# Optimization experiments

Hardware: AMD Instinct MI355X
Metric: run time of the kernel (lower is better)

## Reference

```python
import jax, jax.numpy as jnp
import numpy as np

B, N, K, D = 8, 4096, 8, 256
EPS = 1e-8
LN_EPS = 1e-5


def setup_inputs() -> dict:
    key = jax.random.key(0)
    ks = jax.random.split(key, 9)
    lim_s = float(np.sqrt(6.0 / (K + D)))   # xavier_uniform on (K, D) fan dims
    lim_w = float(np.sqrt(6.0 / (D + D)))   # xavier-ish init for square Linear weights
    return {
        "embeddings": jax.random.normal(ks[0], (B, N, D), jnp.float32),
        "slots_mu": jax.random.uniform(ks[1], (1, K, D), jnp.float32, -lim_s, lim_s),
        "slots_logsigma": jax.random.uniform(ks[2], (1, K, D), jnp.float32, -lim_s, lim_s),
        "mixing_coeffs": jnp.full((1, K), 1.0 / K, jnp.float32),
        "Wq": jax.random.uniform(ks[3], (D, D), jnp.float32, -lim_w, lim_w),
        "Wk": jax.random.uniform(ks[4], (D, D), jnp.float32, -lim_w, lim_w),
        "Wv": jax.random.uniform(ks[5], (D, D), jnp.float32, -lim_w, lim_w),
        "ln_scale": jnp.ones((D,), jnp.float32),
        "ln_bias": jnp.zeros((D,), jnp.float32),
        "noise_init": jax.random.normal(ks[6], (B, K, D), jnp.float32),
        "noise_final": jax.random.normal(ks[7], (B, K, D), jnp.float32),
        "num_iterations": 3,
    }


def _layer_norm(x, scale, bias):
    m = jnp.mean(x, axis=-1, keepdims=True)
    v = jnp.mean((x - m) ** 2, axis=-1, keepdims=True)  # biased var, matches torch LayerNorm
    return (x - m) / jnp.sqrt(v + LN_EPS) * scale + bias


def reference(embeddings, slots_mu, slots_logsigma, mixing_coeffs, Wq, Wk, Wv,
              ln_scale, ln_bias, noise_init, noise_final, num_iterations):
    b, n, d = embeddings.shape
    k = slots_mu.shape[1]
    mix = jnp.broadcast_to(mixing_coeffs, (b, k))               # (B,K)
    mu = jnp.broadcast_to(slots_mu, (b, k, d))                  # (B,K,D)
    sigma = jnp.exp(jnp.broadcast_to(slots_logsigma, (b, k, d)))
    slots = mu + sigma * noise_init                             # slots never updated in loop (faithful)

    x = _layer_norm(embeddings, ln_scale, ln_bias)
    keys = x @ Wk.T                                             # (B,N,D)
    values = x @ Wv.T                                           # (B,N,D)

    log_norm_const = jnp.float32(-0.5 * d * np.log(2.0 * np.pi))
    attn = None
    for _ in range(num_iterations):
        queries = slots @ Wq.T                                  # (B,K,D)
        diff = keys[:, :, None, :] - queries[:, None, :, :]     # (B,N,K,D)
        gll = -0.5 * jnp.sum(diff ** 2 / (sigma[:, None] ** 2 + EPS), axis=-1)  # (B,N,K)
        gll = (log_norm_const
               - 0.5 * jnp.sum(jnp.log(jnp.abs(sigma) + EPS), axis=-1)[:, None, :]
               + gll)
        gll = jnp.clip(gll, -10000.0, 10000.0)
        log_attn = jnp.log(mix + EPS)[:, None, :] + gll         # (B,N,K)
        attn = jax.nn.softmax(log_attn, axis=1)                 # softmax over N
        mu = jnp.einsum('bnk,bnd->bkd', attn, values)           # weighted mean
        diff_v = values[:, :, None, :] - mu[:, None, :, :]      # (B,N,K,D)
        sigma = jnp.einsum('bnk,bnkd->bkd', attn, diff_v ** 2)  # weighted variance
        mix = jnp.sum(attn, axis=1) / n

    sigma = jnp.maximum(jnp.abs(sigma), EPS)
    slots_out = mu + sigma * noise_final
    return slots_out, jnp.transpose(attn, (0, 2, 1))            # (B,K,D), (B,K,N)
```

## Files before the change

### kernel.cpp

```cpp
#include <hip/hip_runtime.h>
#include <math.h>


#define Bd 8
#define Nd 4096
#define Kd 8
#define Dd 256
#define Md (Bd*Nd)
#define NITER 3
#define EPSf 1e-8f
#define LNEPS 1e-5f
#define NCH 64
#define LOGNORM -235.24826450039617f

typedef float f32x4 __attribute__((ext_vector_type(4)));
typedef short bf16x8 __attribute__((ext_vector_type(8)));
typedef unsigned short ushort_t;
typedef unsigned short us4 __attribute__((ext_vector_type(4)));

#define KEYS_OFF 0
#define VALS_OFF (Md*Dd)
#define E_OFF    (2*Md*Dd)
#define Q_OFF    (E_OFF + Bd*Kd*Nd)
#define W_OFF    (Q_OFF + Bd*Kd*Dd)
#define CST_OFF  (W_OFF + Bd*Kd*Dd)
#define MSP_OFF  (CST_OFF + 64)
#define SSP_OFF  (MSP_OFF + Bd*Kd*NCH)
#define PMU_OFF  (SSP_OFF + Bd*Kd*NCH)
#define PS2_OFF  (PMU_OFF + Bd*NCH*Kd*Dd)
#define WH_OFF   (PS2_OFF + Bd*NCH*Kd*Dd)
#define WL_OFF   (WH_OFF + 65536)
#define XH_OFF   (WL_OFF + 65536)
#define XL_OFF   (XH_OFF + Md*Dd/2)
#define WS_TOTAL (XL_OFF + Md*Dd/2)

__device__ __forceinline__ ushort_t f2bf(float f) {
    unsigned u = __float_as_uint(f);
    return (ushort_t)((u + 0x7FFFu + ((u >> 16) & 1u)) >> 16);
}
__device__ __forceinline__ float b2f(ushort_t h) {
    return __uint_as_float(((unsigned)h) << 16);
}
__device__ __forceinline__ void gload_lds16(const void* g, void* l) {
    __builtin_amdgcn_global_load_lds(
        (__attribute__((address_space(1))) void*)g,
        (__attribute__((address_space(3))) void*)l, 16, 0, 0);
}

__global__ __launch_bounds__(256) void k_setup(
        const float* __restrict__ emb, const float* __restrict__ lns,
        const float* __restrict__ lnb, const float* __restrict__ Wk,
        const float* __restrict__ Wv, const float* __restrict__ mu0,
        const float* __restrict__ lsig, const float* __restrict__ nz0,
        const float* __restrict__ Wq, ushort_t* __restrict__ xh,
        ushort_t* __restrict__ xl, ushort_t* __restrict__ Wh,
        ushort_t* __restrict__ Wl, float* __restrict__ qout,
        float* __restrict__ w_ws, float* __restrict__ cst_ws) {
    __shared__ float s_s[256];
    __shared__ float red[256];
    const int bx = blockIdx.x;
    if (bx < 1024) {
        const int tid = threadIdx.x, wave = tid >> 6, lane = tid & 63;
        const int row0 = bx * 32;
        const float4 sc = ((const float4*)lns)[lane];
        const float4 bi = ((const float4*)lnb)[lane];
        for (int rr = 0; rr < 8; ++rr) {
            const int r = row0 + wave * 8 + rr;
            const float4 e4 = ((const float4*)(emb + (size_t)r * Dd))[lane];
            float s = e4.x + e4.y + e4.z + e4.w;
            #pragma unroll
            for (int off = 32; off; off >>= 1) s += __shfl_xor(s, off);
            const float m = s * (1.0f / 256.0f);
            const float dx = e4.x - m, dy = e4.y - m, dz = e4.z - m, dw = e4.w - m;
            float ss = dx * dx + dy * dy + dz * dz + dw * dw;
            #pragma unroll
            for (int off = 32; off; off >>= 1) ss += __shfl_xor(ss, off);
            const float rs = 1.0f / sqrtf(ss * (1.0f / 256.0f) + LNEPS);
            float x[4];
            x[0] = dx * rs * sc.x + bi.x;
            x[1] = dy * rs * sc.y + bi.y;
            x[2] = dz * rs * sc.z + bi.z;
            x[3] = dw * rs * sc.w + bi.w;
            us4 h4, l4;
            #pragma unroll
            for (int j = 0; j < 4; ++j) {
                const ushort_t h = f2bf(x[j]);
                h4[j] = h;
                l4[j] = f2bf(x[j] - b2f(h));
            }
            *(us4*)(xh + (size_t)r * Dd + lane * 4) = h4;
            *(us4*)(xl + (size_t)r * Dd + lane * 4) = l4;
        }
    } else if (bx < 1536) {
        const int r = bx - 1024, d = threadIdx.x;
        const float w = (r < 256) ? Wk[(size_t)r * 256 + d]
                                  : Wv[(size_t)(r - 256) * 256 + d];
        const ushort_t h = f2bf(w);
        Wh[(size_t)r * 256 + d] = h;
        Wl[(size_t)r * 256 + d] = f2bf(w - b2f(h));
    } else {
        const int bk = bx - 1536;
        const int k = bk & 7;
        const int d = threadIdx.x;
        const float sg = expf(lsig[k * 256 + d]);
        s_s[d] = mu0[k * 256 + d] + sg * nz0[(size_t)bk * 256 + d];
        w_ws[(size_t)bk * 256 + d] = 1.0f / (sg * sg + EPSf);
        red[d] = logf(fabsf(sg) + EPSf);
        __syncthreads();
        for (int s = 128; s; s >>= 1) {
            if (d < s) red[d] += red[d + s];
            __syncthreads();
        }
        if (d == 0) cst_ws[bk] = LOGNORM - 0.5f * red[0];
        float acc = 0.0f;
        const float4* Wr = (const float4*)(Wq + (size_t)d * 256);
        const float4* sp = (const float4*)s_s;
        #pragma unroll 8
        for (int j = 0; j < 64; ++j) {
            const float4 w4 = Wr[j], s4 = sp[j];
            acc += w4.x * s4.x + w4.y * s4.y + w4.z * s4.z + w4.w * s4.w;
        }
        qout[(size_t)bk * 256 + d] = acc;
    }
}

__global__ __launch_bounds__(256, 2) void k_gemm(
        const ushort_t* __restrict__ xh, const ushort_t* __restrict__ xl,
        const ushort_t* __restrict__ Wh, const ushort_t* __restrict__ Wl,
        float* __restrict__ keys, float* __restrict__ vals) {
    __shared__ ushort_t Ah[128 * 32], Al[128 * 32];
    __shared__ ushort_t Bh[256 * 32], Bl[256 * 32];
    const int tid = threadIdx.x, lane = tid & 63, wave = tid >> 6;
    const int row0 = blockIdx.x * 128;
    const int cb = blockIdx.y;
    const int wm = wave >> 1, wn = wave & 1;

    f32x4 acc[4][8];
    #pragma unroll
    for (int a = 0; a < 4; ++a)
        #pragma unroll
        for (int b = 0; b < 8; ++b) acc[a][b] = (f32x4)(0.0f);

    for (int jb = 0; jb < 256; jb += 32) {
        #pragma unroll
        for (int i = 0; i < 2; ++i) {
            const int p = tid + i * 256;
            const int r = p >> 2, gp = p & 3;
            const int g = gp ^ ((r >> 1) & 3);
            const size_t goff = (size_t)(row0 + r) * 256 + jb + g * 8;
            gload_lds16(xh + goff, &Ah[p * 8]);
            gload_lds16(xl + goff, &Al[p * 8]);
        }
        #pragma unroll
        for (int i = 0; i < 4; ++i) {
            const int p = (wave * 4 + i) * 64 + lane;
            const int r = p >> 2, gp = p & 3;
            const int g = gp ^ ((r >> 1) & 3);
            const size_t goff = (size_t)(cb * 256 + r) * 256 + jb + g * 8;
            gload_lds16(Wh + goff, &Bh[p * 8]);
            gload_lds16(Wl + goff, &Bl[p * 8]);
        }
        __syncthreads();

        bf16x8 bhf[8], blf[8];
        #pragma unroll
        for (int ni = 0; ni < 8; ++ni) {
            const int c = wn * 128 + ni * 16 + (lane & 15);
            const int g = lane >> 4;
            const int off = c * 32 + ((g ^ ((c >> 1) & 3)) << 3);
            bhf[ni] = *(const bf16x8*)&Bh[off];
            blf[ni] = *(const bf16x8*)&Bl[off];
        }
        #pragma unroll
        for (int mi = 0; mi < 4; ++mi) {
            const int rr = wm * 64 + mi * 16 + (lane & 15);
            const int g = lane >> 4;
            const int off = rr * 32 + ((g ^ ((rr >> 1) & 3)) << 3);
            const bf16x8 ah = *(const bf16x8*)&Ah[off];
            const bf16x8 al = *(const bf16x8*)&Al[off];
            #pragma unroll
            for (int ni = 0; ni < 8; ++ni) {
                acc[mi][ni] = __builtin_amdgcn_mfma_f32_16x16x32_bf16(ah, bhf[ni], acc[mi][ni], 0, 0, 0);
                acc[mi][ni] = __builtin_amdgcn_mfma_f32_16x16x32_bf16(ah, blf[ni], acc[mi][ni], 0, 0, 0);
                acc[mi][ni] = __builtin_amdgcn_mfma_f32_16x16x32_bf16(al, bhf[ni], acc[mi][ni], 0, 0, 0);
            }
        }
        __syncthreads();
    }
    float* outp = (cb == 0) ? keys : vals;
    #pragma unroll
    for (int mi = 0; mi < 4; ++mi) {
        const int rbase = row0 + wm * 64 + mi * 16 + ((lane >> 4) << 2);
        #pragma unroll
        for (int ni = 0; ni < 8; ++ni) {
            const int col = wn * 128 + ni * 16 + (lane & 15);
            #pragma unroll
            for (int rg = 0; rg < 4; ++rg)
                outp[(size_t)(rbase + rg) * Dd + col] = acc[mi][ni][rg];
        }
    }
}

__global__ __launch_bounds__(512, 4) void k_fuse(
        const float* __restrict__ keys, const float* __restrict__ vals,
        const float* __restrict__ q_ws, const float* __restrict__ w_ws,
        const float* __restrict__ cst_ws, float* __restrict__ e_glob,
        float* __restrict__ msp, float* __restrict__ ssp,
        float* __restrict__ pmu, float* __restrict__ ps2, const int last) {
    __shared__ float buf[16384];
    __shared__ float e_s[8][64];
    const int tid = threadIdx.x, lane = tid & 63, wv = tid >> 6;
    const int b = blockIdx.x >> 6, chunk = blockIdx.x & 63;
    const int n0 = chunk * 64;
    const int wvu = __builtin_amdgcn_readfirstlane(wv);

    const float* kbase = keys + ((size_t)b * Nd + n0) * Dd;
    #pragma unroll
    for (int i = 0; i < 8; ++i) {
        const int p = i * 512 + tid;
        const int row = p >> 6, gp = p & 63;
        const int g = gp ^ row;
        gload_lds16(kbase + (size_t)row * Dd + g * 4, &buf[p * 4]);
    }
    __syncthreads();

    const float4* qk = (const float4*)(q_ws + ((size_t)b * Kd + wvu) * Dd);
    const float4* wk = (const float4*)(w_ws + ((size_t)b * Kd + wvu) * Dd);
    const float* krow = &buf[lane * 256];
    float ax = 0.f, ay = 0.f, az = 0.f, aw = 0.f;
    #pragma unroll 8
    for (int g = 0; g < 64; ++g) {
        const float4 k4 = *(const float4*)&krow[(g ^ lane) * 4];
        const float4 q4 = qk[g];
        const float4 w4 = wk[g];
        float t;
        t = k4.x - q4.x; ax += t * t * w4.x;
        t = k4.y - q4.y; ay += t * t * w4.y;
        t = k4.z - q4.z; az += t * t * w4.z;
        t = k4.w - q4.w; aw += t * t * w4.w;
    }
    float gv = cst_ws[b * Kd + wvu] - 0.5f * ((ax + ay) + (az + aw));
    gv = fminf(fmaxf(gv, -10000.0f), 10000.0f);
    float m = gv;
    #pragma unroll
    for (int off = 32; off; off >>= 1) m = fmaxf(m, __shfl_xor(m, off));
    const float e = expf(gv - m);
    float ssum = e;
    #pragma unroll
    for (int off = 32; off; off >>= 1) ssum += __shfl_xor(ssum, off);
    e_s[wv][lane] = e;
    if (last) e_glob[((size_t)(b * Kd + wvu)) * Nd + n0 + lane] = e;
    if (lane == 0) {
        msp[(b * Kd + wvu) * NCH + chunk] = m;
        ssp[(b * Kd + wvu) * NCH + chunk] = ssum;
    }
    __syncthreads();

    const float* vbase = vals + ((size_t)b * Nd + n0) * Dd;
    #pragma unroll
    for (int i = 0; i < 8; ++i) {
        const int p = i * 512 + tid;
        gload_lds16(vbase + (size_t)p * 4, &buf[p * 4]);
    }
    __syncthreads();

    float4 mu4 = {0.f, 0.f, 0.f, 0.f}, s24 = {0.f, 0.f, 0.f, 0.f};
    #pragma unroll 8
    for (int n = 0; n < 64; ++n) {
        const float4 v = *(const float4*)&buf[n * 256 + lane * 4];
        const float a = e_s[wv][n];
        mu4.x += a * v.x; mu4.y += a * v.y; mu4.z += a * v.z; mu4.w += a * v.w;
        s24.x += a * v.x * v.x; s24.y += a * v.y * v.y;
        s24.z += a * v.z * v.z; s24.w += a * v.w * v.w;
    }
    const size_t o = (((size_t)(b * NCH + chunk)) * Kd + wv) * Dd + lane * 4;
    *(float4*)(pmu + o) = mu4;
    *(float4*)(ps2 + o) = s24;
}

__global__ __launch_bounds__(256) void k_prep(
        const float* __restrict__ msp, const float* __restrict__ ssp,
        const float* __restrict__ pmu, const float* __restrict__ ps2,
        float* __restrict__ w_ws, float* __restrict__ cst_ws,
        const float* __restrict__ nzf, float* __restrict__ slots_out,
        const float* __restrict__ e_glob, float* __restrict__ attn,
        const int last) {
    __shared__ float wS[64];
    __shared__ float aS[64];
    __shared__ float sinv_s;
    __shared__ float4 muP[4][64];
    __shared__ float4 s2P[4][64];
    const int bk = blockIdx.x;
    const int b = bk >> 3, k = bk & 7;
    const int tid = threadIdx.x, lane = tid & 63, grp = tid >> 6;
    if (grp == 0) {
        const float m_c = msp[bk * NCH + lane];
        const float s_c = ssp[bk * NCH + lane];
        float M = m_c;
        #pragma unroll
        for (int off = 32; off; off >>= 1) M = fmaxf(M, __shfl_xor(M, off));
        const float wc = expf(m_c - M);
        float S = wc * s_c;
        #pragma unroll
        for (int off = 32; off; off >>= 1) S += __shfl_xor(S, off);
        wS[lane] = wc;
        aS[lane] = wc / S;
        if (lane == 0) sinv_s = 1.0f / S;
    }
    __syncthreads();
    float4 am = {0.f, 0.f, 0.f, 0.f}, a2 = {0.f, 0.f, 0.f, 0.f};
    #pragma unroll
    for (int i = 0; i < 16; ++i) {
        const int c = grp * 16 + i;
        const float wc = wS[c];
        const size_t o = (((size_t)(b * NCH + c)) * Kd + k) * Dd + lane * 4;
        const float4 pm = *(const float4*)(pmu + o);
        const float4 p2 = *(const float4*)(ps2 + o);
        am.x += wc * pm.x; am.y += wc * pm.y; am.z += wc * pm.z; am.w += wc * pm.w;
        a2.x += wc * p2.x; a2.y += wc * p2.y; a2.z += wc * p2.z; a2.w += wc * p2.w;
    }
    muP[grp][lane] = am;
    s2P[grp][lane] = a2;
    __syncthreads();
    if (grp == 0) {
        const float sinv = sinv_s;
        float4 mu, E2;
        mu.x = (muP[0][lane].x + muP[1][lane].x + muP[2][lane].x + muP[3][lane].x) * sinv;
        mu.y = (muP[0][lane].y + muP[1][lane].y + muP[2][lane].y + muP[3][lane].y) * sinv;
        mu.z = (muP[0][lane].z + muP[1][lane].z + muP[2][lane].z + muP[3][lane].z) * sinv;
        mu.w = (muP[0][lane].w + muP[1][lane].w + muP[2][lane].w + muP[3][lane].w) * sinv;
        E2.x = (s2P[0][lane].x + s2P[1][lane].x + s2P[2][lane].x + s2P[3][lane].x) * sinv;
        E2.y = (s2P[0][lane].y + s2P[1][lane].y + s2P[2][lane].y + s2P[3][lane].y) * sinv;
        E2.z = (s2P[0][lane].z + s2P[1][lane].z + s2P[2][lane].z + s2P[3][lane].z) * sinv;
        E2.w = (s2P[0][lane].w + s2P[1][lane].w + s2P[2][lane].w + s2P[3][lane].w) * sinv;
        float4 sg;
        sg.x = E2.x - mu.x * mu.x; sg.y = E2.y - mu.y * mu.y;
        sg.z = E2.z - mu.z * mu.z; sg.w = E2.w - mu.w * mu.w;
        float4 wout;
        wout.x = 1.0f / (sg.x * sg.x + EPSf); wout.y = 1.0f / (sg.y * sg.y + EPSf);
        wout.z = 1.0f / (sg.z * sg.z + EPSf); wout.w = 1.0f / (sg.w * sg.w + EPSf);
        *(float4*)(w_ws + (size_t)bk * Dd + lane * 4) = wout;
        const float4 nz = *(const float4*)(nzf + (size_t)bk * Dd + lane * 4);
        float4 so;
        so.x = mu.x + fmaxf(fabsf(sg.x), EPSf) * nz.x;
        so.y = mu.y + fmaxf(fabsf(sg.y), EPSf) * nz.y;
        so.z = mu.z + fmaxf(fabsf(sg.z), EPSf) * nz.z;
        so.w = mu.w + fmaxf(fabsf(sg.w), EPSf) * nz.w;
        *(float4*)(slots_out + (size_t)bk * Dd + lane * 4) = so;
        float lsum = logf(fabsf(sg.x) + EPSf) + logf(fabsf(sg.y) + EPSf)
                   + logf(fabsf(sg.z) + EPSf) + logf(fabsf(sg.w) + EPSf);
        #pragma unroll
        for (int off = 32; off; off >>= 1) lsum += __shfl_xor(lsum, off);
        if (lane == 0) cst_ws[bk] = LOGNORM - 0.5f * lsum;
    }
    if (last) {
        const float4* erow = (const float4*)(e_glob + (size_t)bk * Nd);
        float4* arow = (float4*)(attn + (size_t)bk * Nd);
        #pragma unroll
        for (int i = 0; i < 4; ++i) {
            const int idx = tid + i * 256;
            const float4 e4 = erow[idx];
            const float a = aS[idx >> 4];
            float4 o4;
            o4.x = e4.x * a; o4.y = e4.y * a; o4.z = e4.z * a; o4.w = e4.w * a;
            arow[idx] = o4;
        }
    }
}

extern "C" void kernel_launch(void* const* d_in, const int* in_sizes, int n_in,
                              void* d_out, int out_size, void* d_ws, size_t ws_size,
                              hipStream_t stream) {
    const float* emb  = (const float*)d_in[0];
    const float* mu0  = (const float*)d_in[1];
    const float* lsig = (const float*)d_in[2];
    const float* Wq   = (const float*)d_in[4];
    const float* Wk   = (const float*)d_in[5];
    const float* Wv   = (const float*)d_in[6];
    const float* lns  = (const float*)d_in[7];
    const float* lnb  = (const float*)d_in[8];
    const float* nz0  = (const float*)d_in[9];
    const float* nzf  = (const float*)d_in[10];

    float* ws    = (float*)d_ws;
    float* out   = (float*)d_out;
    float* keys  = ws + KEYS_OFF;
    float* vals  = ws + VALS_OFF;
    float* eglob = ws + E_OFF;
    float* qws   = ws + Q_OFF;
    float* wws   = ws + W_OFF;
    float* cstw  = ws + CST_OFF;
    float* msp   = ws + MSP_OFF;
    float* ssp   = ws + SSP_OFF;
    float* pmu   = ws + PMU_OFF;
    float* ps2   = ws + PS2_OFF;
    ushort_t* Whp = (ushort_t*)(ws + WH_OFF);
    ushort_t* Wlp = (ushort_t*)(ws + WL_OFF);
    ushort_t* xhp = (ushort_t*)(ws + XH_OFF);
    ushort_t* xlp = (ushort_t*)(ws + XL_OFF);
    float* attn = out + Bd * Kd * Dd;

    k_setup<<<1600, 256, 0, stream>>>(emb, lns, lnb, Wk, Wv, mu0, lsig, nz0,
                                      Wq, xhp, xlp, Whp, Wlp, qws, wws, cstw);
    k_gemm<<<dim3(256, 2), 256, 0, stream>>>(xhp, xlp, Whp, Wlp, keys, vals);
    for (int it = 0; it < NITER; ++it) {
        const int last = (it == NITER - 1);
        k_fuse<<<512, 512, 0, stream>>>(keys, vals, qws, wws, cstw, eglob,
                                        msp, ssp, pmu, ps2, last);
        k_prep<<<64, 256, 0, stream>>>(msp, ssp, pmu, ps2, wws, cstw, nzf,
                                       out, eglob, attn, last);
    }
    (void)in_sizes; (void)n_in; (void)out_size; (void)ws_size;
}
```

Baseline: 208.2 us.

## Split per-slot reduction kernel across D-slices with atomic log-sum accumulation

The reduction kernel that combines per-chunk softmax partials into mu, sigma and the log-normalizer now runs as 512 blocks of 512 threads instead of 64 blocks of 256. Each block handles one 32-wide D slice of a (b,k) slot and reduces chunks with wave shuffles. Because the log-sum constant now spans several blocks, it is accumulated with atomicAdd into a per-iteration buffer that setup zeroes, and the fuse kernel reads it. Slot outputs are written only on the last iteration. This raises parallelism in a kernel that previously filled few CUs, at the cost of atomics and repeated per-block max/scale computation.

```diff
diff --git a/kernel.cpp b/kernel.cpp
--- a/kernel.cpp
+++ b/kernel.cpp
@@ -24,7 +24,8 @@
 #define Q_OFF    (E_OFF + Bd*Kd*Nd)
 #define W_OFF    (Q_OFF + Bd*Kd*Dd)
 #define CST_OFF  (W_OFF + Bd*Kd*Dd)
-#define MSP_OFF  (CST_OFF + 64)
+#define CSTA_OFF (CST_OFF + 64)
+#define MSP_OFF  (CSTA_OFF + 192)
 #define SSP_OFF  (MSP_OFF + Bd*Kd*NCH)
 #define PMU_OFF  (SSP_OFF + Bd*Kd*NCH)
 #define PS2_OFF  (PMU_OFF + Bd*NCH*Kd*Dd)
@@ -55,7 +56,8 @@
         const float* __restrict__ Wq, ushort_t* __restrict__ xh,
         ushort_t* __restrict__ xl, ushort_t* __restrict__ Wh,
         ushort_t* __restrict__ Wl, float* __restrict__ qout,
-        float* __restrict__ w_ws, float* __restrict__ cst_ws) {
+        float* __restrict__ w_ws, float* __restrict__ cst_ws,
+        float* __restrict__ cst_acc) {
     __shared__ float s_s[256];
     __shared__ float red[256];
     const int bx = blockIdx.x;
@@ -102,6 +104,7 @@
         const int bk = bx - 1536;
         const int k = bk & 7;
         const int d = threadIdx.x;
+        if (d < 3) cst_acc[d * 64 + bk] = 0.0f;
         const float sg = expf(lsig[k * 256 + d]);
         s_s[d] = mu0[k * 256 + d] + sg * nz0[(size_t)bk * 256 + d];
         w_ws[(size_t)bk * 256 + d] = 1.0f / (sg * sg + EPSf);
@@ -204,9 +207,10 @@
 __global__ __launch_bounds__(512, 4) void k_fuse(
         const float* __restrict__ keys, const float* __restrict__ vals,
         const float* __restrict__ q_ws, const float* __restrict__ w_ws,
-        const float* __restrict__ cst_ws, float* __restrict__ e_glob,
-        float* __restrict__ msp, float* __restrict__ ssp,
-        float* __restrict__ pmu, float* __restrict__ ps2, const int last) {
+        const float* __restrict__ cst_ws, const float* __restrict__ cst_acc,
+        float* __restrict__ e_glob, float* __restrict__ msp,
+        float* __restrict__ ssp, float* __restrict__ pmu,
+        float* __restrict__ ps2, const int it, const int last) {
     __shared__ float buf[16384];
     __shared__ float e_s[8][64];
     const int tid = threadIdx.x, lane = tid & 63, wv = tid >> 6;
@@ -224,8 +228,11 @@
     }
     __syncthreads();
 
-    const float4* qk = (const float4*)(q_ws + ((size_t)b * Kd + wvu) * Dd);
-    const float4* wk = (const float4*)(w_ws + ((size_t)b * Kd + wvu) * Dd);
+    const int bkf = b * Kd + wvu;
+    const float4* qk = (const float4*)(q_ws + (size_t)bkf * Dd);
+    const float4* wk = (const float4*)(w_ws + (size_t)bkf * Dd);
+    const float cstv = (it == 0) ? cst_ws[bkf]
+                     : fmaf(-0.5f, cst_acc[(it - 1) * 64 + bkf], LOGNORM);
     const float* krow = &buf[lane * 256];
     float ax = 0.f, ay = 0.f, az = 0.f, aw = 0.f;
     #pragma unroll 8
@@ -239,7 +246,7 @@
         t = k4.z - q4.z; az += t * t * w4.z;
         t = k4.w - q4.w; aw += t * t * w4.w;
     }
-    float gv = cst_ws[b * Kd + wvu] - 0.5f * ((ax + ay) + (az + aw));
+    float gv = cstv - 0.5f * ((ax + ay) + (az + aw));
     gv = fminf(fmaxf(gv, -10000.0f), 10000.0f);
     float m = gv;
     #pragma unroll
@@ -249,10 +256,10 @@
     #pragma unroll
     for (int off = 32; off; off >>= 1) ssum += __shfl_xor(ssum, off);
     e_s[wv][lane] = e;
-    if (last) e_glob[((size_t)(b * Kd + wvu)) * Nd + n0 + lane] = e;
+    if (last) e_glob[((size_t)bkf) * Nd + n0 + lane] = e;
     if (lane == 0) {
-        msp[(b * Kd + wvu) * NCH + chunk] = m;
-        ssp[(b * Kd + wvu) * NCH + chunk] = ssum;
+        msp[bkf * NCH + chunk] = m;
+        ssp[bkf * NCH + chunk] = ssum;
     }
     __syncthreads();
 
@@ -278,22 +285,21 @@
     *(float4*)(ps2 + o) = s24;
 }
 
-__global__ __launch_bounds__(256) void k_prep(
+__global__ __launch_bounds__(512) void k_red(
         const float* __restrict__ msp, const float* __restrict__ ssp,
         const float* __restrict__ pmu, const float* __restrict__ ps2,
-        float* __restrict__ w_ws, float* __restrict__ cst_ws,
+        float* __restrict__ w_ws, float* __restrict__ cst_acc,
         const float* __restrict__ nzf, float* __restrict__ slots_out,
         const float* __restrict__ e_glob, float* __restrict__ attn,
-        const int last) {
-    __shared__ float wS[64];
+        const int it, const int last) {
     __shared__ float aS[64];
-    __shared__ float sinv_s;
-    __shared__ float4 muP[4][64];
-    __shared__ float4 s2P[4][64];
-    const int bk = blockIdx.x;
+    __shared__ f32x4 redm[8][8], red2[8][8];
+    const int bx = blockIdx.x;
+    const int bk = bx >> 3, ds = bx & 7;
     const int b = bk >> 3, k = bk & 7;
-    const int tid = threadIdx.x, lane = tid & 63, grp = tid >> 6;
-    if (grp == 0) {
+    const int tid = threadIdx.x, lane = tid & 63, wv = tid >> 6;
+
+    if (wv == 0) {
         const float m_c = msp[bk * NCH + lane];
         const float s_c = ssp[bk * NCH + lane];
         float M = m_c;
@@ -303,68 +309,72 @@
         float S = wc * s_c;
         #pragma unroll
         for (int off = 32; off; off >>= 1) S += __shfl_xor(S, off);
-        wS[lane] = wc;
         aS[lane] = wc / S;
-        if (lane == 0) sinv_s = 1.0f / S;
     }
     __syncthreads();
-    float4 am = {0.f, 0.f, 0.f, 0.f}, a2 = {0.f, 0.f, 0.f, 0.f};
-    #pragma unroll
-    for (int i = 0; i < 16; ++i) {
-        const int c = grp * 16 + i;
-        const float wc = wS[c];
-        const size_t o = (((size_t)(b * NCH + c)) * Kd + k) * Dd + lane * 4;
-        const float4 pm = *(const float4*)(pmu + o);
-        const float4 p2 = *(const float4*)(ps2 + o);
-        am.x += wc * pm.x; am.y += wc * pm.y; am.z += wc * pm.z; am.w += wc * pm.w;
-        a2.x += wc * p2.x; a2.y += wc * p2.y; a2.z += wc * p2.z; a2.w += wc * p2.w;
-    }
-    muP[grp][lane] = am;
-    s2P[grp][lane] = a2;
+
+    const int c0 = tid >> 3, f = tid & 7;
+    const size_t base = (((size_t)(b * NCH + c0)) * Kd + k) * Dd + ds * 32 + f * 4;
+    const float a = aS[c0];
+    const float4 pm = *(const float4*)(pmu + base);
+    const float4 p2 = *(const float4*)(ps2 + base);
+    f32x4 m4 = {a * pm.x, a * pm.y, a * pm.z, a * pm.w};
+    f32x4 e4 = {a * p2.x, a * p2.y, a * p2.z, a * p2.w};
+    #pragma unroll
+    for (int off = 8; off < 64; off <<= 1) {
+        m4.x += __shfl_xor(m4.x, off); m4.y += __shfl_xor(m4.y, off);
+        m4.z += __shfl_xor(m4.z, off); m4.w += __shfl_xor(m4.w, off);
+        e4.x += __shfl_xor(e4.x, off); e4.y += __shfl_xor(e4.y, off);
+        e4.z += __shfl_xor(e4.z, off); e4.w += __shfl_xor(e4.w, off);
+    }
+    if (lane < 8) { redm[wv][lane] = m4; red2[wv][lane] = e4; }
     __syncthreads();
-    if (grp == 0) {
-        const float sinv = sinv_s;
-        float4 mu, E2;
-        mu.x = (muP[0][lane].x + muP[1][lane].x + muP[2][lane].x + muP[3][lane].x) * sinv;
-        mu.y = (muP[0][lane].y + muP[1][lane].y + muP[2][lane].y + muP[3][lane].y) * sinv;
-        mu.z = (muP[0][lane].z + muP[1][lane].z + muP[2][lane].z + muP[3][lane].z) * sinv;
-        mu.w = (muP[0][lane].w + muP[1][lane].w + muP[2][lane].w + muP[3][lane].w) * sinv;
-        E2.x = (s2P[0][lane].x + s2P[1][lane].x + s2P[2][lane].x + s2P[3][lane].x) * sinv;
-        E2.y = (s2P[0][lane].y + s2P[1][lane].y + s2P[2][lane].y + s2P[3][lane].y) * sinv;
-        E2.z = (s2P[0][lane].z + s2P[1][lane].z + s2P[2][lane].z + s2P[3][lane].z) * sinv;
-        E2.w = (s2P[0][lane].w + s2P[1][lane].w + s2P[2][lane].w + s2P[3][lane].w) * sinv;
-        float4 sg;
-        sg.x = E2.x - mu.x * mu.x; sg.y = E2.y - mu.y * mu.y;
-        sg.z = E2.z - mu.z * mu.z; sg.w = E2.w - mu.w * mu.w;
-        float4 wout;
-        wout.x = 1.0f / (sg.x * sg.x + EPSf); wout.y = 1.0f / (sg.y * sg.y + EPSf);
-        wout.z = 1.0f / (sg.z * sg.z + EPSf); wout.w = 1.0f / (sg.w * sg.w + EPSf);
-        *(float4*)(w_ws + (size_t)bk * Dd + lane * 4) = wout;
-        const float4 nz = *(const float4*)(nzf + (size_t)bk * Dd + lane * 4);
-        float4 so;
-        so.x = mu.x + fmaxf(fabsf(sg.x), EPSf) * nz.x;
-        so.y = mu.y + fmaxf(fabsf(sg.y), EPSf) * nz.y;
-        so.z = mu.z + fmaxf(fabsf(sg.z), EPSf) * nz.z;
-        so.w = mu.w + fmaxf(fabsf(sg.w), EPSf) * nz.w;
-        *(float4*)(slots_out + (size_t)bk * Dd + lane * 4) = so;
-        float lsum = logf(fabsf(sg.x) + EPSf) + logf(fabsf(sg.y) + EPSf)
-                   + logf(fabsf(sg.z) + EPSf) + logf(fabsf(sg.w) + EPSf);
-        #pragma unroll
-        for (int off = 32; off; off >>= 1) lsum += __shfl_xor(lsum, off);
-        if (lane == 0) cst_ws[bk] = LOGNORM - 0.5f * lsum;
-    }
-    if (last) {
-        const float4* erow = (const float4*)(e_glob + (size_t)bk * Nd);
-        float4* arow = (float4*)(attn + (size_t)bk * Nd);
-        #pragma unroll
-        for (int i = 0; i < 4; ++i) {
-            const int idx = tid + i * 256;
-            const float4 e4 = erow[idx];
-            const float a = aS[idx >> 4];
-            float4 o4;
-            o4.x = e4.x * a; o4.y = e4.y * a; o4.z = e4.z * a; o4.w = e4.w * a;
-            arow[idx] = o4;
-        }
+
+    if (wv == 0) {
+        f32x4 mm = redm[lane >> 3][lane & 7];
+        f32x4 ee = red2[lane >> 3][lane & 7];
+        #pragma unroll
+        for (int off = 8; off < 64; off <<= 1) {
+            mm.x += __shfl_xor(mm.x, off); mm.y += __shfl_xor(mm.y, off);
+            mm.z += __shfl_xor(mm.z, off); mm.w += __shfl_xor(mm.w, off);
+            ee.x += __shfl_xor(ee.x, off); ee.y += __shfl_xor(ee.y, off);
+            ee.z += __shfl_xor(ee.z, off); ee.w += __shfl_xor(ee.w, off);
+        }
+        if (lane < 8) {
+            const int d0 = ds * 32 + lane * 4;
+            const float sgx = ee.x - mm.x * mm.x;
+            const float sgy = ee.y - mm.y * mm.y;
+            const float sgz = ee.z - mm.z * mm.z;
+            const float sgw = ee.w - mm.w * mm.w;
+            float4 wout;
+            wout.x = 1.0f / (sgx * sgx + EPSf);
+            wout.y = 1.0f / (sgy * sgy + EPSf);
+            wout.z = 1.0f / (sgz * sgz + EPSf);
+            wout.w = 1.0f / (sgw * sgw + EPSf);
+            *(float4*)(w_ws + (size_t)bk * Dd + d0) = wout;
+            if (last) {
+                const float4 nz = *(const float4*)(nzf + (size_t)bk * Dd + d0);
+                float4 so;
+                so.x = mm.x + fmaxf(fabsf(sgx), EPSf) * nz.x;
+                so.y = mm.y + fmaxf(fabsf(sgy), EPSf) * nz.y;
+                so.z = mm.z + fmaxf(fabsf(sgz), EPSf) * nz.z;
+                so.w = mm.w + fmaxf(fabsf(sgw), EPSf) * nz.w;
+                *(float4*)(slots_out + (size_t)bk * Dd + d0) = so;
+            }
+            float ls = logf(fabsf(sgx) + EPSf) + logf(fabsf(sgy) + EPSf)
+                     + logf(fabsf(sgz) + EPSf) + logf(fabsf(sgw) + EPSf);
+            #pragma unroll
+            for (int off = 1; off < 8; off <<= 1) ls += __shfl_xor(ls, off);
+            if (lane == 0) atomicAdd(cst_acc + it * 64 + bk, ls);
+        }
+    }
+    if (last && tid < 128) {
+        const int idx = ds * 128 + tid;
+        const float4 ev = ((const float4*)(e_glob + (size_t)bk * Nd))[idx];
+        const float s = aS[idx >> 4];
+        float4 o4;
+        o4.x = ev.x * s; o4.y = ev.y * s; o4.z = ev.z * s; o4.w = ev.w * s;
+        ((float4*)(attn + (size_t)bk * Nd))[idx] = o4;
     }
 }
 
@@ -390,6 +400,7 @@
     float* qws   = ws + Q_OFF;
     float* wws   = ws + W_OFF;
     float* cstw  = ws + CST_OFF;
+    float* csta  = ws + CSTA_OFF;
     float* msp   = ws + MSP_OFF;
     float* ssp   = ws + SSP_OFF;
     float* pmu   = ws + PMU_OFF;
@@ -401,14 +412,15 @@
     float* attn = out + Bd * Kd * Dd;
 
     k_setup<<<1600, 256, 0, stream>>>(emb, lns, lnb, Wk, Wv, mu0, lsig, nz0,
-                                      Wq, xhp, xlp, Whp, Wlp, qws, wws, cstw);
+                                      Wq, xhp, xlp, Whp, Wlp, qws, wws, cstw,
+                                      csta);
     k_gemm<<<dim3(256, 2), 256, 0, stream>>>(xhp, xlp, Whp, Wlp, keys, vals);
     for (int it = 0; it < NITER; ++it) {
         const int last = (it == NITER - 1);
-        k_fuse<<<512, 512, 0, stream>>>(keys, vals, qws, wws, cstw, eglob,
-                                        msp, ssp, pmu, ps2, last);
-        k_prep<<<64, 256, 0, stream>>>(msp, ssp, pmu, ps2, wws, cstw, nzf,
-                                       out, eglob, attn, last);
+        k_fuse<<<512, 512, 0, stream>>>(keys, vals, qws, wws, cstw, csta,
+                                        eglob, msp, ssp, pmu, ps2, it, last);
+        k_red<<<512, 512, 0, stream>>>(msp, ssp, pmu, ps2, wws, csta, nzf,
+                                       out, eglob, attn, it, last);
     }
     (void)in_sizes; (void)n_in; (void)out_size; (void)ws_size;
 }
```

After: 215.3 us. 3.4% more time.

## Read values directly from global in fused kernel; widen prep kernel to 1024 threads

Applied to the files above, without the earlier changes.

In the fused attention kernel, the LDS staging of the value tile and its two barriers are removed, and each wave reads values straight from global memory with coalesced float4 loads. The reduction kernel grows from 256 to 1024 threads per block, so each of 16 groups reduces 4 chunk partials instead of 4 groups reducing 16, and the attention normalization becomes a single float4 per thread. The aim is to cut barrier and LDS-copy latency and to expose more parallelism in the small 64-block prep kernel. The cost is that the 8 waves of a block each reread the same value tile from global or L2 instead of sharing one LDS copy, and the final cross-group sum is longer.

```diff
diff --git a/kernel.cpp b/kernel.cpp
--- a/kernel.cpp
+++ b/kernel.cpp
@@ -254,20 +254,12 @@
         msp[(b * Kd + wvu) * NCH + chunk] = m;
         ssp[(b * Kd + wvu) * NCH + chunk] = ssum;
     }
-    __syncthreads();
-
-    const float* vbase = vals + ((size_t)b * Nd + n0) * Dd;
-    #pragma unroll
-    for (int i = 0; i < 8; ++i) {
-        const int p = i * 512 + tid;
-        gload_lds16(vbase + (size_t)p * 4, &buf[p * 4]);
-    }
-    __syncthreads();
 
     float4 mu4 = {0.f, 0.f, 0.f, 0.f}, s24 = {0.f, 0.f, 0.f, 0.f};
+    const float* vbase = vals + ((size_t)b * Nd + n0) * Dd + lane * 4;
     #pragma unroll 8
     for (int n = 0; n < 64; ++n) {
-        const float4 v = *(const float4*)&buf[n * 256 + lane * 4];
+        const float4 v = *(const float4*)(vbase + (size_t)n * Dd);
         const float a = e_s[wv][n];
         mu4.x += a * v.x; mu4.y += a * v.y; mu4.z += a * v.z; mu4.w += a * v.w;
         s24.x += a * v.x * v.x; s24.y += a * v.y * v.y;
@@ -278,7 +270,7 @@
     *(float4*)(ps2 + o) = s24;
 }
 
-__global__ __launch_bounds__(256) void k_prep(
+__global__ __launch_bounds__(1024) void k_prep(
         const float* __restrict__ msp, const float* __restrict__ ssp,
         const float* __restrict__ pmu, const float* __restrict__ ps2,
         float* __restrict__ w_ws, float* __restrict__ cst_ws,
@@ -288,8 +280,8 @@
     __shared__ float wS[64];
     __shared__ float aS[64];
     __shared__ float sinv_s;
-    __shared__ float4 muP[4][64];
-    __shared__ float4 s2P[4][64];
+    __shared__ float4 muP[16][64];
+    __shared__ float4 s2P[16][64];
     const int bk = blockIdx.x;
     const int b = bk >> 3, k = bk & 7;
     const int tid = threadIdx.x, lane = tid & 63, grp = tid >> 6;
@@ -310,8 +302,8 @@
     __syncthreads();
     float4 am = {0.f, 0.f, 0.f, 0.f}, a2 = {0.f, 0.f, 0.f, 0.f};
     #pragma unroll
-    for (int i = 0; i < 16; ++i) {
-        const int c = grp * 16 + i;
+    for (int i = 0; i < 4; ++i) {
+        const int c = grp * 4 + i;
         const float wc = wS[c];
         const size_t o = (((size_t)(b * NCH + c)) * Kd + k) * Dd + lane * 4;
         const float4 pm = *(const float4*)(pmu + o);
@@ -324,15 +316,16 @@
     __syncthreads();
     if (grp == 0) {
         const float sinv = sinv_s;
-        float4 mu, E2;
-        mu.x = (muP[0][lane].x + muP[1][lane].x + muP[2][lane].x + muP[3][lane].x) * sinv;
-        mu.y = (muP[0][lane].y + muP[1][lane].y + muP[2][lane].y + muP[3][lane].y) * sinv;
-        mu.z = (muP[0][lane].z + muP[1][lane].z + muP[2][lane].z + muP[3][lane].z) * sinv;
-        mu.w = (muP[0][lane].w + muP[1][lane].w + muP[2][lane].w + muP[3][lane].w) * sinv;
-        E2.x = (s2P[0][lane].x + s2P[1][lane].x + s2P[2][lane].x + s2P[3][lane].x) * sinv;
-        E2.y = (s2P[0][lane].y + s2P[1][lane].y + s2P[2][lane].y + s2P[3][lane].y) * sinv;
-        E2.z = (s2P[0][lane].z + s2P[1][lane].z + s2P[2][lane].z + s2P[3][lane].z) * sinv;
-        E2.w = (s2P[0][lane].w + s2P[1][lane].w + s2P[2][lane].w + s2P[3][lane].w) * sinv;
+        float4 mu = {0.f, 0.f, 0.f, 0.f}, E2 = {0.f, 0.f, 0.f, 0.f};
+        #pragma unroll
+        for (int gi = 0; gi < 16; ++gi) {
+            const float4 pm = muP[gi][lane];
+            const float4 p2 = s2P[gi][lane];
+            mu.x += pm.x; mu.y += pm.y; mu.z += pm.z; mu.w += pm.w;
+            E2.x += p2.x; E2.y += p2.y; E2.z += p2.z; E2.w += p2.w;
+        }
+        mu.x *= sinv; mu.y *= sinv; mu.z *= sinv; mu.w *= sinv;
+        E2.x *= sinv; E2.y *= sinv; E2.z *= sinv; E2.w *= sinv;
         float4 sg;
         sg.x = E2.x - mu.x * mu.x; sg.y = E2.y - mu.y * mu.y;
         sg.z = E2.z - mu.z * mu.z; sg.w = E2.w - mu.w * mu.w;
@@ -354,17 +347,11 @@
         if (lane == 0) cst_ws[bk] = LOGNORM - 0.5f * lsum;
     }
     if (last) {
-        const float4* erow = (const float4*)(e_glob + (size_t)bk * Nd);
-        float4* arow = (float4*)(attn + (size_t)bk * Nd);
-        #pragma unroll
-        for (int i = 0; i < 4; ++i) {
-            const int idx = tid + i * 256;
-            const float4 e4 = erow[idx];
-            const float a = aS[idx >> 4];
-            float4 o4;
-            o4.x = e4.x * a; o4.y = e4.y * a; o4.z = e4.z * a; o4.w = e4.w * a;
-            arow[idx] = o4;
-        }
+        const float4 e4 = ((const float4*)(e_glob + (size_t)bk * Nd))[tid];
+        const float a = aS[tid >> 4];
+        float4 o4;
+        o4.x = e4.x * a; o4.y = e4.y * a; o4.z = e4.z * a; o4.w = e4.w * a;
+        ((float4*)(attn + (size_t)bk * Nd))[tid] = o4;
     }
 }
 
@@ -407,8 +394,8 @@
         const int last = (it == NITER - 1);
         k_fuse<<<512, 512, 0, stream>>>(keys, vals, qws, wws, cstw, eglob,
                                         msp, ssp, pmu, ps2, last);
-        k_prep<<<64, 256, 0, stream>>>(msp, ssp, pmu, ps2, wws, cstw, nzf,
-                                       out, eglob, attn, last);
+        k_prep<<<64, 1024, 0, stream>>>(msp, ssp, pmu, ps2, wws, cstw, nzf,
+                                        out, eglob, attn, last);
     }
     (void)in_sizes; (void)n_in; (void)out_size; (void)ws_size;
 }
```

Result: no change. 210.5 us (+1.1%).
